# Optimization experiments

Hardware: AMD Instinct MI355X
Metric: run time of the kernel (lower is better)

## Reference

```python
import jax, jax.numpy as jnp
import numpy as np

EPS = 1e-5


def _layernorm(x, w, b):
    mu = jnp.mean(x, axis=-1, keepdims=True)
    xc = x - mu
    var = jnp.mean(xc * xc, axis=-1, keepdims=True)
    return xc * jax.lax.rsqrt(var + EPS) * w + b


def _s5_ssm(u, lam_re, lam_im, log_step, B_re, B_im, C_re, C_im, Dvec):
    # u: [B,L,D]; diagonal complex SSM with ZOH discretization + associative scan
    Lam = lam_re + 1j * lam_im                      # [P]
    step = jnp.exp(log_step)                        # [P]
    Abar = jnp.exp(Lam * step)                      # [P]
    Bbar = ((Abar - 1.0) / Lam)[:, None] * (B_re + 1j * B_im)  # [P,D]
    Bu = jnp.einsum('bld,pd->blp', u.astype(jnp.complex64), Bbar)  # [B,L,P]
    A_el = jnp.broadcast_to(Abar, Bu.shape)

    def binop(e1, e2):
        a1, b1 = e1
        a2, b2 = e2
        return a1 * a2, a2 * b1 + b2

    _, xs = jax.lax.associative_scan(binop, (A_el, Bu), axis=1)  # [B,L,P] complex
    y = jnp.einsum('blp,dp->bld', xs, C_re + 1j * C_im).real + Dvec * u
    return y


def _s5_block(x, an_w, an_b, lam_re, lam_im, log_step, B_re, B_im, C_re, C_im,
              Dvec, fn_w, fn_b, Wenc, Wdec):
    fx = _layernorm(x, an_w, an_b)
    s = _s5_ssm(fx, lam_re, lam_im, log_step, B_re, B_im, C_re, C_im, Dvec)
    z = jax.nn.gelu(s, approximate=False) + fx
    fy = _layernorm(z, fn_w, fn_b)
    h = fy @ Wenc.T                                  # [B,L,2D]
    a, g = jnp.split(h, 2, axis=-1)                  # GEGLU
    return (a * jax.nn.gelu(g, approximate=False)) @ Wdec.T + fy


def setup_inputs() -> dict:
    D = 1048   # d_model
    P = 1048   # state_dim
    NL = 3
    Bsz, L = 4, 4096
    key = jax.random.key(0)
    ks = jax.random.split(key, 20)
    f32 = jnp.float32
    inp = {}
    inp['x'] = jax.random.normal(ks[0], (Bsz, L, 1), f32)
    inp['enc_w'] = jax.random.normal(ks[1], (D, 1), f32)
    inp['enc_b'] = jnp.zeros((D,), f32)
    inp['norm_w'] = jnp.ones((NL, D), f32)
    inp['norm_b'] = jnp.zeros((NL, D), f32)
    inp['attn_norm_w'] = jnp.ones((NL, D), f32)
    inp['attn_norm_b'] = jnp.zeros((NL, D), f32)
    inp['ff_norm_w'] = jnp.ones((NL, D), f32)
    inp['ff_norm_b'] = jnp.zeros((NL, D), f32)
    # stable diagonal dynamics: Re(Lambda) < 0
    inp['lam_re'] = -0.5 * jax.random.uniform(ks[2], (NL, P), f32) - 0.05
    inp['lam_im'] = np.float32(np.pi) * jax.random.normal(ks[3], (NL, P), f32)
    lo, hi = np.float32(np.log(1e-3)), np.float32(np.log(1e-1))
    inp['log_step'] = lo + (hi - lo) * jax.random.uniform(ks[4], (NL, P), f32)
    sB = np.float32(1.0 / np.sqrt(D))
    sC = np.float32(1.0 / np.sqrt(P))
    inp['B_re'] = sB * jax.random.normal(ks[5], (NL, P, D), f32)
    inp['B_im'] = sB * jax.random.normal(ks[6], (NL, P, D), f32)
    inp['C_re'] = sC * jax.random.normal(ks[7], (NL, D, P), f32)
    inp['C_im'] = sC * jax.random.normal(ks[8], (NL, D, P), f32)
    inp['Dvec'] = jax.random.normal(ks[9], (NL, D), f32)
    sW = np.float32(1.0 / np.sqrt(D))
    inp['Wenc'] = sW * jax.random.normal(ks[10], (NL, 2 * D, D), f32)
    inp['Wdec'] = sW * jax.random.normal(ks[11], (NL, D, D), f32)
    inp['head_w'] = sW * jax.random.normal(ks[12], (1, D), f32)
    inp['head_b'] = jnp.zeros((1,), f32)
    return inp


def reference(x, enc_w, enc_b, norm_w, norm_b, attn_norm_w, attn_norm_b,
              ff_norm_w, ff_norm_b, lam_re, lam_im, log_step, B_re, B_im,
              C_re, C_im, Dvec, Wenc, Wdec, head_w, head_b):
    h = x @ enc_w.T + enc_b                          # [B,L,D]
    n_layers = norm_w.shape[0]
    for i in range(n_layers):                        # small fixed loop over layers
        z = _layernorm(h, norm_w[i], norm_b[i])      # prenorm
        z = _s5_block(z, attn_norm_w[i], attn_norm_b[i], lam_re[i], lam_im[i],
                      log_step[i], B_re[i], B_im[i], C_re[i], C_im[i],
                      Dvec[i], ff_norm_w[i], ff_norm_b[i], Wenc[i], Wdec[i])
        h = h + z                                    # residual (dropout = identity in eval)
    pooled = jnp.mean(h, axis=1)                     # [B,D]
    y = (pooled @ head_w.T + head_b).squeeze(-1)     # [B]
    return y
```

## Files before the change

kernel.cpp:

```cpp
#include <hip/hip_runtime.h>
#include <hip/hip_bf16.h>
#include <cstddef>

typedef __hip_bfloat16 bf16;

#define D_MODEL 1048
#define P_DIM   1048
#define NLAYER  3
#define BSZ     4
#define LSEQ    4096
#define BL      (BSZ*LSEQ)
#define BLD     ((size_t)BL*D_MODEL)
#define KP      1056
#define NP      1152
#define BLA     ((size_t)BL*KP)
#define NPKP    ((size_t)NP*KP)

#define NC      64
#define CL      (LSEQ/NC)
#define NSCAN   (BSZ*NC*P_DIM)
#define P2      (P_DIM/2)
#define NSCAN2  (BSZ*NC*P2)

typedef __attribute__((ext_vector_type(8))) short short8;
typedef __attribute__((ext_vector_type(4))) float f32x4;

#define BM 256
#define BN 128
#define TK 32
#define ASH (BM*TK)
#define BSH (BN*TK)
#define SLOT1 (ASH + BSH)
#define SLOT2 (ASH + 2*BSH)
#define KSTEPS  (KP/TK)
#define NG2   ((BL/BM)*(NP/BN))

__device__ __forceinline__ float gelu_f(float x) {
    return 0.5f * x * (1.f + erff(x * 0.70710678118654752f));
}

__device__ __forceinline__ void tile_coords(int id, int& m0, int& n0) {
    int xcd  = id & 7;
    int slot = id >> 3;
    int xg   = slot / 9;
    int j    = slot - xg*9;
    m0 = (xg*8 + xcd) * BM;
    n0 = j * BN;
}

__device__ __forceinline__ void stageA256(
    const bf16* __restrict__ src, int row0, int k0, short* lds, int tid)
{
#pragma unroll
    for (int c0 = 0; c0 < 2; ++c0) {
        int c = tid + 512*c0;
        int r = c >> 2;
        int col = ((c ^ (r >> 1)) & 3) * 8;
        __builtin_amdgcn_global_load_lds(
            (const __attribute__((address_space(1))) void*)(src + (size_t)(row0 + r)*KP + k0 + col),
            (__attribute__((address_space(3))) void*)(lds + c*8), 16, 0, 0);
    }
}
__device__ __forceinline__ void stageB128(
    const bf16* __restrict__ src, int row0, int k0, short* lds, int tid)
{
    int r = tid >> 2;
    int col = ((tid ^ (r >> 1)) & 3) * 8;
    __builtin_amdgcn_global_load_lds(
        (const __attribute__((address_space(1))) void*)(src + (size_t)(row0 + r)*KP + k0 + col),
        (__attribute__((address_space(3))) void*)(lds + tid*8), 16, 0, 0);
}

__device__ __forceinline__ void mfma_step1(
    const short* As, const short* Ws, f32x4 (&acc)[4][4],
    int wm, int wn, int row_in, int qs)
{
    short8 a[4], b[4];
#pragma unroll
    for (int i = 0; i < 4; ++i) {
        a[i] = *(const short8*)&As[(wm + i*16 + row_in)*TK + qs];
        b[i] = *(const short8*)&Ws[(wn + i*16 + row_in)*TK + qs];
    }
#pragma unroll
    for (int i = 0; i < 4; ++i)
#pragma unroll
        for (int j = 0; j < 4; ++j)
            acc[i][j] = __builtin_amdgcn_mfma_f32_16x16x32_bf16(a[i], b[j], acc[i][j], 0, 0, 0);
}

__device__ __forceinline__ void mfma_step2(
    const short* As, const short* W0s, const short* W1s,
    f32x4 (&acc0)[4][4], f32x4 (&acc1)[4][4],
    int wm, int wn, int row_in, int qs)
{
    short8 a[4], b0[4], b1[4];
#pragma unroll
    for (int i = 0; i < 4; ++i) {
        a[i]  = *(const short8*)&As [(wm + i*16 + row_in)*TK + qs];
        b0[i] = *(const short8*)&W0s[(wn + i*16 + row_in)*TK + qs];
        b1[i] = *(const short8*)&W1s[(wn + i*16 + row_in)*TK + qs];
    }
#pragma unroll
    for (int i = 0; i < 4; ++i)
#pragma unroll
        for (int j = 0; j < 4; ++j) {
            acc0[i][j] = __builtin_amdgcn_mfma_f32_16x16x32_bf16(a[i], b0[j], acc0[i][j], 0, 0, 0);
            acc1[i][j] = __builtin_amdgcn_mfma_f32_16x16x32_bf16(a[i], b1[j], acc1[i][j], 0, 0, 0);
        }
}

template <int NPASS>
__device__ __forceinline__ void kloop1(
    const bf16* __restrict__ A0, const bf16* __restrict__ W0,
    const bf16* __restrict__ A1, const bf16* __restrict__ W1,
    int m0, int n0, short* sm,
    f32x4 (&acc)[4][4], int tid, int wm, int wn, int row_in, int qs)
{
    const int NST = NPASS*KSTEPS;
#define STAGE1(t) { int _t = (t); \
        const bf16* _A = (NPASS == 2 && _t >= KSTEPS) ? A1 : A0; \
        const bf16* _W = (NPASS == 2 && _t >= KSTEPS) ? W1 : W0; \
        int _kk = (NPASS == 2 && _t >= KSTEPS) ? _t - KSTEPS : _t; \
        short* _b = sm + (_t & 3)*SLOT1; \
        stageA256(_A, m0, _kk*TK, _b, tid); \
        stageB128(_W, n0, _kk*TK, _b + ASH, tid); }
    STAGE1(0); STAGE1(1); STAGE1(2);
    for (int s = 0; s < NST; ++s) {
        if (s < NST - 2)       asm volatile("s_waitcnt vmcnt(6)" ::: "memory");
        else if (s == NST - 2) asm volatile("s_waitcnt vmcnt(3)" ::: "memory");
        else                   asm volatile("s_waitcnt vmcnt(0)" ::: "memory");
        __builtin_amdgcn_s_barrier();
        if (s < NST - 3) STAGE1(s + 3);
        short* base = sm + (s & 3)*SLOT1;
        __builtin_amdgcn_s_setprio(1);
        mfma_step1(base, base + ASH, acc, wm, wn, row_in, qs);
        __builtin_amdgcn_s_setprio(0);
    }
#undef STAGE1
}

template <int MODE>
__global__ __launch_bounds__(512, 2) void gemm2_k(
    const bf16* __restrict__ A, const bf16* __restrict__ W0,
    const bf16* __restrict__ W1,
    bf16* __restrict__ O0, bf16* __restrict__ O1, int N)
{
    __shared__ __align__(16) short sm[4*SLOT2];
    const int tid  = threadIdx.x;
    int m0, n0;
    tile_coords(blockIdx.x, m0, n0);
    const int wave = tid >> 6, lane = tid & 63;
    const int wm = (wave >> 1) * 64, wn = (wave & 1) * 64;
    const int row_in = lane & 15;
    const int qs = (((lane >> 4) ^ (lane >> 1)) & 3) * 8;

    f32x4 acc0[4][4] = {};
    f32x4 acc1[4][4] = {};

#define STAGE2(t) { int _t = (t); \
        short* _b = sm + (_t & 3)*SLOT2; \
        stageA256(A,  m0, _t*TK, _b, tid); \
        stageB128(W0, n0, _t*TK, _b + ASH, tid); \
        stageB128(W1, n0, _t*TK, _b + ASH + BSH, tid); }
    STAGE2(0); STAGE2(1); STAGE2(2);
    for (int s = 0; s < KSTEPS; ++s) {
        if (s < KSTEPS - 2)       asm volatile("s_waitcnt vmcnt(8)" ::: "memory");
        else if (s == KSTEPS - 2) asm volatile("s_waitcnt vmcnt(4)" ::: "memory");
        else                      asm volatile("s_waitcnt vmcnt(0)" ::: "memory");
        __builtin_amdgcn_s_barrier();
        if (s < KSTEPS - 3) STAGE2(s + 3);
        short* base = sm + (s & 3)*SLOT2;
        __builtin_amdgcn_s_setprio(1);
        mfma_step2(base, base + ASH, base + ASH + BSH, acc0, acc1, wm, wn, row_in, qs);
        __builtin_amdgcn_s_setprio(0);
    }
#undef STAGE2

    const int quad = lane >> 4;
#pragma unroll
    for (int i = 0; i < 4; ++i) {
#pragma unroll
        for (int j = 0; j < 4; ++j) {
            int n = n0 + wn + j*16 + row_in;
#pragma unroll
            for (int r = 0; r < 4; ++r) {
                int m = m0 + wm + i*16 + quad*4 + r;
                size_t o = (size_t)m*KP + n;
                if (MODE == 0) {
                    if (n < N)        { O0[o] = __float2bfloat16(acc0[i][j][r]);
                                        O1[o] = __float2bfloat16(acc1[i][j][r]); }
                    else if (n < KP)  { O0[o] = __float2bfloat16(0.f);
                                        O1[o] = __float2bfloat16(0.f); }
                } else {
                    if (n < N)        O0[o] = __float2bfloat16(acc0[i][j][r] * gelu_f(acc1[i][j][r]));
                    else if (n < KP)  O0[o] = __float2bfloat16(0.f);
                }
            }
        }
    }
}

__global__ __launch_bounds__(512, 2) void gemmC_k(
    const bf16* __restrict__ A0, const bf16* __restrict__ W0,
    const bf16* __restrict__ A1, const bf16* __restrict__ W1,
    const bf16* __restrict__ fx, const float* __restrict__ dv,
    bf16* __restrict__ O, int N)
{
    __shared__ __align__(16) short sm[4*SLOT1];
    const int tid  = threadIdx.x;
    int m0, n0;
    tile_coords(blockIdx.x, m0, n0);
    const int wave = tid >> 6, lane = tid & 63;
    const int wm = (wave >> 1) * 64, wn = (wave & 1) * 64;
    const int row_in = lane & 15;
    const int qs = (((lane >> 4) ^ (lane >> 1)) & 3) * 8;

    f32x4 acc[4][4] = {};
    kloop1<2>(A0, W0, A1, W1, m0, n0, sm, acc, tid, wm, wn, row_in, qs);

    const int quad = lane >> 4;
#pragma unroll
    for (int i = 0; i < 4; ++i) {
#pragma unroll
        for (int j = 0; j < 4; ++j) {
            int n = n0 + wn + j*16 + row_in;
#pragma unroll
            for (int r = 0; r < 4; ++r) {
                int m = m0 + wm + i*16 + quad*4 + r;
                size_t o = (size_t)m*KP + n;
                if (n < N) {
                    float f = __bfloat162float(fx[o]);
                    float t = acc[i][j][r] + dv[n]*f;
                    O[o] = __float2bfloat16(gelu_f(t) + f);
                } else if (n < KP) {
                    O[o] = __float2bfloat16(0.f);
                }
            }
        }
    }
}

__global__ __launch_bounds__(512, 2) void gemmD_k(
    const bf16* __restrict__ A, const bf16* __restrict__ W,
    const bf16* __restrict__ fy, float* __restrict__ h, int N)
{
    __shared__ __align__(16) short sm[4*SLOT1];
    const int tid  = threadIdx.x;
    int m0, n0;
    tile_coords(blockIdx.x, m0, n0);
    const int wave = tid >> 6, lane = tid & 63;
    const int wm = (wave >> 1) * 64, wn = (wave & 1) * 64;
    const int row_in = lane & 15;
    const int qs = (((lane >> 4) ^ (lane >> 1)) & 3) * 8;

    f32x4 acc[4][4] = {};
    kloop1<1>(A, W, nullptr, nullptr, m0, n0, sm, acc, tid, wm, wn, row_in, qs);

    const int quad = lane >> 4;
#pragma unroll
    for (int i = 0; i < 4; ++i) {
#pragma unroll
        for (int j = 0; j < 4; ++j) {
            int n = n0 + wn + j*16 + row_in;
            if (n >= N) continue;
#pragma unroll
            for (int r = 0; r < 4; ++r) {
                int m = m0 + wm + i*16 + quad*4 + r;
                float f = __bfloat162float(fy[(size_t)m*KP + n]);
                h[(size_t)m*D_MODEL + n] += acc[i][j][r] + f;
            }
        }
    }
}

__global__ __launch_bounds__(256) void convw5_k(
    const float* __restrict__ s0, const float* __restrict__ s1,
    const float* __restrict__ s2, const float* __restrict__ s3,
    const float* __restrict__ s4, bf16* __restrict__ dst)
{
    size_t i = (size_t)blockIdx.x*256 + threadIdx.x;
    if (i >= NPKP) return;
    int z = blockIdx.z;
    const float* src = (z == 0) ? s0 : (z == 1) ? s1 : (z == 2) ? s2 : (z == 3) ? s3 : s4;
    float scale = (z == 1) ? -1.f : 1.f;
    int n = (int)(i / KP), k = (int)(i - (size_t)n*KP);
    float v = (n < D_MODEL && k < D_MODEL) ? scale*src[(size_t)n*D_MODEL + k] : 0.f;
    dst[(size_t)z*NPKP + i] = __float2bfloat16(v);
}

__device__ __forceinline__ float2 block_reduce2(float a, float b) {
    __syncthreads();
    for (int off = 32; off; off >>= 1) {
        a += __shfl_down(a, off, 64);
        b += __shfl_down(b, off, 64);
    }
    __shared__ float sa[4], sb[4];
    int lane = threadIdx.x & 63, wv = threadIdx.x >> 6;
    if (lane == 0) { sa[wv] = a; sb[wv] = b; }
    __syncthreads();
    if (threadIdx.x == 0) {
        sa[0] = sa[0]+sa[1]+sa[2]+sa[3];
        sb[0] = sb[0]+sb[1]+sb[2]+sb[3];
    }
    __syncthreads();
    return make_float2(sa[0], sb[0]);
}

template <int ENC>
__global__ __launch_bounds__(256) void ln2x_k(
    const float* __restrict__ xin,
    const float* __restrict__ ew, const float* __restrict__ eb,
    float* __restrict__ hbuf,
    const float* __restrict__ w1, const float* __restrict__ bb1,
    const float* __restrict__ w2, const float* __restrict__ bb2,
    bf16* __restrict__ y)
{
    const size_t row = blockIdx.x;
    float v[5];
    float s = 0.f, ss = 0.f;
    int i = 0;
    if (ENC) {
        float xv = xin[row];
        float* hr = hbuf + row * D_MODEL;
        for (int d = threadIdx.x; d < KP; d += 256, ++i) {
            float t = 0.f;
            if (d < D_MODEL) { t = xv*ew[d] + eb[d]; hr[d] = t; }
            v[i] = t; s += t; ss += t*t;
        }
    } else {
        const float* xr = hbuf + row * D_MODEL;
        for (int d = threadIdx.x; d < KP; d += 256, ++i) {
            float t = (d < D_MODEL) ? xr[d] : 0.f;
            v[i] = t; s += t; ss += t*t;
        }
    }
    float2 r = block_reduce2(s, ss);
    float mu  = r.x * (1.f/D_MODEL);
    float var = r.y * (1.f/D_MODEL) - mu*mu;
    float inv = rsqrtf(var + 1e-5f);
    s = 0.f; ss = 0.f; i = 0;
    for (int d = threadIdx.x; d < KP; d += 256, ++i) {
        float z = (d < D_MODEL) ? (v[i]-mu)*inv*w1[d] + bb1[d] : 0.f;
        v[i] = z; s += z; ss += z*z;
    }
    r = block_reduce2(s, ss);
    mu  = r.x * (1.f/D_MODEL);
    var = r.y * (1.f/D_MODEL) - mu*mu;
    inv = rsqrtf(var + 1e-5f);
    bf16* yr = y + row * KP;
    i = 0;
    for (int d = threadIdx.x; d < KP; d += 256, ++i) {
        float o = (d < D_MODEL) ? (v[i]-mu)*inv*w2[d] + bb2[d] : 0.f;
        yr[d] = __float2bfloat16(o);
    }
}

__global__ __launch_bounds__(256) void ln_k(
    const bf16* __restrict__ x, const float* __restrict__ w,
    const float* __restrict__ b, bf16* __restrict__ y)
{
    const size_t row = blockIdx.x;
    const bf16* xr = x + row * KP;
    float v[5];
    float s = 0.f, ss = 0.f;
    int i = 0;
    for (int d = threadIdx.x; d < KP; d += 256, ++i) {
        float t = (d < D_MODEL) ? __bfloat162float(xr[d]) : 0.f;
        v[i] = t; s += t; ss += t*t;
    }
    float2 r = block_reduce2(s, ss);
    float mu  = r.x * (1.f/D_MODEL);
    float var = r.y * (1.f/D_MODEL) - mu*mu;
    float inv = rsqrtf(var + 1e-5f);
    bf16* yr = y + row * KP;
    i = 0;
    for (int d = threadIdx.x; d < KP; d += 256, ++i) {
        float o = (d < D_MODEL) ? (v[i]-mu)*inv*w[d] + b[d] : 0.f;
        yr[d] = __float2bfloat16(o);
    }
}

__global__ __launch_bounds__(256) void prep_k(
    const float* __restrict__ lam_re, const float* __restrict__ lam_im,
    const float* __restrict__ log_step,
    const float* __restrict__ B_re, const float* __restrict__ B_im,
    bf16* __restrict__ bbar_re, bf16* __restrict__ bbar_im,
    float* __restrict__ abar)
{
    size_t idx = (size_t)blockIdx.x*256 + threadIdx.x;
    if (idx >= NPKP) return;
    int p = (int)(idx / KP);
    int d = (int)(idx - (size_t)p*KP);
    if (p >= P_DIM || d >= D_MODEL) {
        bbar_re[idx] = __float2bfloat16(0.f);
        bbar_im[idx] = __float2bfloat16(0.f);
        return;
    }
    float lr = lam_re[p], li = lam_im[p];
    float st = expf(log_step[p]);
    float er = expf(lr*st);
    float ar = er * cosf(li*st);
    float ai = er * sinf(li*st);
    if (d == 0) { abar[p] = ar; abar[P_DIM + p] = ai; }
    float den = lr*lr + li*li;
    float xr = ar - 1.f, xi = ai;
    float cr = (xr*lr + xi*li) / den;
    float ci = (xi*lr - xr*li) / den;
    float br = B_re[(size_t)p*D_MODEL + d], bi = B_im[(size_t)p*D_MODEL + d];
    bbar_re[idx] = __float2bfloat16(cr*br - ci*bi);
    bbar_im[idx] = __float2bfloat16(cr*bi + ci*br);
}

__device__ __forceinline__ float2 bf2f(unsigned int u) {
    unsigned int lo = u << 16, hi = u & 0xffff0000u;
    float2 r;
    r.x = __uint_as_float(lo);
    r.y = __uint_as_float(hi);
    return r;
}
__device__ __forceinline__ unsigned int f2bf2(float a, float b) {
    bf16 ba = __float2bfloat16(a), bb = __float2bfloat16(b);
    unsigned short ua = *(unsigned short*)&ba, ub = *(unsigned short*)&bb;
    return (unsigned int)ua | ((unsigned int)ub << 16);
}

__global__ __launch_bounds__(256) void scan_partial_k(
    const unsigned int* __restrict__ ur, const unsigned int* __restrict__ ui,
    const float* __restrict__ abar,
    float* __restrict__ sum_re, float* __restrict__ sum_im)
{
    int idx = blockIdx.x*256 + threadIdx.x;
    if (idx >= NSCAN2) return;
    int p2 = idx % P2;
    int rest = idx / P2;
    int c = rest % NC, b = rest / NC;
    int p = 2*p2;
    float ar0 = abar[p],   ai0 = abar[P_DIM + p];
    float ar1 = abar[p+1], ai1 = abar[P_DIM + p + 1];
    size_t base = (((size_t)b*LSEQ + (size_t)c*CL)*KP + p) >> 1;
    float s0r = 0.f, s0i = 0.f, s1r = 0.f, s1i = 0.f;
    for (int i = 0; i < CL; ++i) {
        size_t o = base + (size_t)i*(KP/2);
        float2 br = bf2f(ur[o]);
        float2 bi = bf2f(ui[o]);
        float n0r = fmaf(ar0, s0r, fmaf(-ai0, s0i, br.x));
        float n0i = fmaf(ar0, s0i, fmaf( ai0, s0r, bi.x));
        float n1r = fmaf(ar1, s1r, fmaf(-ai1, s1i, br.y));
        float n1i = fmaf(ar1, s1i, fmaf( ai1, s1r, bi.y));
        s0r = n0r; s0i = n0i; s1r = n1r; s1i = n1i;
    }
    size_t so = ((size_t)b*NC + c)*P_DIM + p;
    *(float2*)&sum_re[so] = make_float2(s0r, s1r);
    *(float2*)&sum_im[so] = make_float2(s0i, s1i);
}

__global__ __launch_bounds__(256) void scan_carry_k(
    const float* __restrict__ sum_re, const float* __restrict__ sum_im,
    const float* __restrict__ abar,
    float* __restrict__ car_re, float* __restrict__ car_im)
{
    int idx = blockIdx.x*256 + threadIdx.x;
    if (idx >= BSZ*P_DIM) return;
    int p = idx % P_DIM, b = idx / P_DIM;
    float cr = abar[p], ci = abar[P_DIM + p];
#pragma unroll
    for (int s = 0; s < 6; ++s) {
        float nr = cr*cr - ci*ci;
        float ni = 2.f*cr*ci;
        cr = nr; ci = ni;
    }
    float xre = 0.f, xim = 0.f;
    size_t base = (size_t)b*NC*P_DIM + p;
    for (int c = 0; c < NC; ++c) {
        size_t o = base + (size_t)c*P_DIM;
        car_re[o] = xre; car_im[o] = xim;
        float sre = sum_re[o], sim = sum_im[o];
        float nr = fmaf(cr, xre, fmaf(-ci, xim, sre));
        float ni = fmaf(cr, xim, fmaf( ci, xre, sim));
        xre = nr; xim = ni;
    }
}

__global__ __launch_bounds__(256) void scan_apply_k(
    unsigned int* __restrict__ ur, unsigned int* __restrict__ ui,
    const float* __restrict__ abar,
    const float* __restrict__ car_re, const float* __restrict__ car_im)
{
    int idx = blockIdx.x*256 + threadIdx.x;
    if (idx >= NSCAN2) return;
    int p2 = idx % P2;
    int rest = idx / P2;
    int c = rest % NC, b = rest / NC;
    int p = 2*p2;
    float ar0 = abar[p],   ai0 = abar[P_DIM + p];
    float ar1 = abar[p+1], ai1 = abar[P_DIM + p + 1];
    size_t co = ((size_t)b*NC + c)*P_DIM + p;
    float2 c_r = *(const float2*)&car_re[co];
    float2 c_i = *(const float2*)&car_im[co];
    float x0r = c_r.x, x0i = c_i.x, x1r = c_r.y, x1i = c_i.y;
    size_t base = (((size_t)b*LSEQ + (size_t)c*CL)*KP + p) >> 1;
    for (int i = 0; i < CL; ++i) {
        size_t o = base + (size_t)i*(KP/2);
        float2 br = bf2f(ur[o]);
        float2 bi = bf2f(ui[o]);
        float n0r = fmaf(ar0, x0r, fmaf(-ai0, x0i, br.x));
        float n0i = fmaf(ar0, x0i, fmaf( ai0, x0r, bi.x));
        float n1r = fmaf(ar1, x1r, fmaf(-ai1, x1i, br.y));
        float n1i = fmaf(ar1, x1i, fmaf( ai1, x1r, bi.y));
        x0r = n0r; x0i = n0i; x1r = n1r; x1i = n1i;
        ur[o] = f2bf2(x0r, x1r);
        ui[o] = f2bf2(x0i, x1i);
    }
}

__global__ void head_init_k(float* out, const float* hb)
{
    if (threadIdx.x < BSZ) out[threadIdx.x] = hb[0];
}

__global__ __launch_bounds__(256) void head_k(
    const float* __restrict__ h, const float* __restrict__ hw,
    float* __restrict__ out)
{
    int b = blockIdx.x;
    int chunk = blockIdx.y;
    const float* hb = h + ((size_t)b*LSEQ + (size_t)chunk*64)*D_MODEL;
    float s = 0.f;
    for (int l = 0; l < 64; ++l) {
        const float* hr = hb + (size_t)l*D_MODEL;
        for (int d = threadIdx.x; d < D_MODEL; d += 256)
            s += hr[d]*hw[d];
    }
    for (int off = 32; off; off >>= 1) s += __shfl_down(s, off, 64);
    __shared__ float sm[4];
    int lane = threadIdx.x & 63, wv = threadIdx.x >> 6;
    if (lane == 0) sm[wv] = s;
    __syncthreads();
    if (threadIdx.x == 0)
        atomicAdd(out + b, (sm[0]+sm[1]+sm[2]+sm[3]) * (1.f/LSEQ));
}

extern "C" void kernel_launch(void* const* d_in, const int* in_sizes, int n_in,
                              void* d_out, int out_size, void* d_ws, size_t ws_size,
                              hipStream_t stream)
{
    const float* x          = (const float*)d_in[0];
    const float* enc_w      = (const float*)d_in[1];
    const float* enc_b      = (const float*)d_in[2];
    const float* norm_w     = (const float*)d_in[3];
    const float* norm_b     = (const float*)d_in[4];
    const float* attn_w     = (const float*)d_in[5];
    const float* attn_b     = (const float*)d_in[6];
    const float* ff_w       = (const float*)d_in[7];
    const float* ff_b       = (const float*)d_in[8];
    const float* lam_re     = (const float*)d_in[9];
    const float* lam_im     = (const float*)d_in[10];
    const float* log_step   = (const float*)d_in[11];
    const float* B_re       = (const float*)d_in[12];
    const float* B_im       = (const float*)d_in[13];
    const float* C_re       = (const float*)d_in[14];
    const float* C_im       = (const float*)d_in[15];
    const float* Dvec       = (const float*)d_in[16];
    const float* Wenc       = (const float*)d_in[17];
    const float* Wdec       = (const float*)d_in[18];
    const float* head_w     = (const float*)d_in[19];
    const float* head_b     = (const float*)d_in[20];
    float* out = (float*)d_out;

    float* h    = (float*)d_ws;
    bf16*  b1   = (bf16*)(h + BLD);
    bf16*  b2   = b1 + BLA;
    bf16*  b3   = b2 + BLA;
    bf16*  b4   = b3 + BLA;
    bf16*  wbr  = b4 + BLA;
    bf16*  wbi  = wbr + NPKP;
    bf16*  w5   = wbi + NPKP;
    bf16*  wcr  = w5;
    bf16*  wci  = w5 + NPKP;
    bf16*  wea  = w5 + 2*NPKP;
    bf16*  weg  = w5 + 3*NPKP;
    bf16*  wd   = w5 + 4*NPKP;
    float* abar = (float*)(w5 + 5*NPKP);
    float* sum_re = abar + 2*P_DIM;
    float* sum_im = sum_re + NSCAN;
    float* car_re = sum_im + NSCAN;
    float* car_im = car_re + NSCAN;

    const int CV   = (int)((NPKP + 255)/256);
    const int SC_G = (NSCAN2 + 255)/256;
    const size_t pd = (size_t)P_DIM*D_MODEL;

    for (int i = 0; i < NLAYER; ++i) {
        prep_k<<<CV, 256, 0, stream>>>(
            lam_re + i*P_DIM, lam_im + i*P_DIM, log_step + i*P_DIM,
            B_re + i*pd, B_im + i*pd, wbr, wbi, abar);
        const float* WencA = Wenc + (size_t)i*2*pd;
        const float* WencG = WencA + pd;
        convw5_k<<<dim3(CV,1,5), 256, 0, stream>>>(
            C_re + i*pd, C_im + i*pd, WencA, WencG, Wdec + i*pd, w5);

        if (i == 0)
            ln2x_k<1><<<BL, 256, 0, stream>>>(x, enc_w, enc_b, h,
                norm_w + i*D_MODEL, norm_b + i*D_MODEL,
                attn_w + i*D_MODEL, attn_b + i*D_MODEL, b2);
        else
            ln2x_k<0><<<BL, 256, 0, stream>>>(nullptr, nullptr, nullptr, h,
                norm_w + i*D_MODEL, norm_b + i*D_MODEL,
                attn_w + i*D_MODEL, attn_b + i*D_MODEL, b2);

        gemm2_k<0><<<NG2, 512, 0, stream>>>(b2, wbr, wbi, b1, b3, P_DIM);

        scan_partial_k<<<SC_G, 256, 0, stream>>>((unsigned int*)b1, (unsigned int*)b3,
                                                 abar, sum_re, sum_im);
        scan_carry_k<<<(BSZ*P_DIM + 255)/256, 256, 0, stream>>>(sum_re, sum_im, abar, car_re, car_im);
        scan_apply_k<<<SC_G, 256, 0, stream>>>((unsigned int*)b1, (unsigned int*)b3,
                                               abar, car_re, car_im);

        gemmC_k<<<NG2, 512, 0, stream>>>(b1, wcr, b3, wci, b2, Dvec + i*D_MODEL, b4, D_MODEL);

        ln_k<<<BL, 256, 0, stream>>>(b4, ff_w + i*D_MODEL, ff_b + i*D_MODEL, b1);

        gemm2_k<1><<<NG2, 512, 0, stream>>>(b1, wea, weg, b2, nullptr, D_MODEL);

        gemmD_k<<<NG2, 512, 0, stream>>>(b2, wd, b1, h, D_MODEL);
    }

    head_init_k<<<1, 64, 0, stream>>>(out, head_b);
    head_k<<<dim3(BSZ, 64), 256, 0, stream>>>(h, head_w, out);
}
```

Before: 2.012 ms.

## Restructure GEMM k-loops into double-k, two-buffer pipelines with interleaved LDS reads

Rewrites the main loops of the three GEMM kernels. Each iteration now consumes two 32-wide k-slices held in one of two LDS buffer groups, and LDS fragment reads are split into halves interleaved with MFMA groups behind extra barriers. New global-to-LDS copies for the next pair of slices are issued mid-iteration, with a separate tail for the odd 33rd slice. The launch-bounds minimum of two blocks per CU is dropped, giving the compiler more register freedom at possible cost in occupancy, and the added barriers may cost synchronisation overhead.

```diff
diff --git a/kernel.cpp b/kernel.cpp
--- a/kernel.cpp
+++ b/kernel.cpp
@@ -27,13 +27,13 @@
 
 #define BM 256
 #define BN 128
-#define TK 32
-#define ASH (BM*TK)
-#define BSH (BN*TK)
-#define SLOT1 (ASH + BSH)
-#define SLOT2 (ASH + 2*BSH)
-#define KSTEPS  (KP/TK)
+#define TKS 32
+#define ASL (BM*TKS)
+#define BSL (BN*TKS)
+#define KSTEPS 33
 #define NG2   ((BL/BM)*(NP/BN))
+
+#define BAR() asm volatile("s_barrier" ::: "memory")
 
 __device__ __forceinline__ float gelu_f(float x) {
     return 0.5f * x * (1.f + erff(x * 0.70710678118654752f));
@@ -48,7 +48,7 @@
     n0 = j * BN;
 }
 
-__device__ __forceinline__ void stageA256(
+__device__ __forceinline__ void stageA(
     const bf16* __restrict__ src, int row0, int k0, short* lds, int tid)
 {
 #pragma unroll
@@ -61,7 +61,7 @@
             (__attribute__((address_space(3))) void*)(lds + c*8), 16, 0, 0);
     }
 }
-__device__ __forceinline__ void stageB128(
+__device__ __forceinline__ void stageB(
     const bf16* __restrict__ src, int row0, int k0, short* lds, int tid)
 {
     int r = tid >> 2;
@@ -71,81 +71,20 @@
         (__attribute__((address_space(3))) void*)(lds + tid*8), 16, 0, 0);
 }
 
-__device__ __forceinline__ void mfma_step1(
-    const short* As, const short* Ws, f32x4 (&acc)[4][4],
-    int wm, int wn, int row_in, int qs)
-{
-    short8 a[4], b[4];
-#pragma unroll
-    for (int i = 0; i < 4; ++i) {
-        a[i] = *(const short8*)&As[(wm + i*16 + row_in)*TK + qs];
-        b[i] = *(const short8*)&Ws[(wn + i*16 + row_in)*TK + qs];
-    }
-#pragma unroll
-    for (int i = 0; i < 4; ++i)
-#pragma unroll
-        for (int j = 0; j < 4; ++j)
-            acc[i][j] = __builtin_amdgcn_mfma_f32_16x16x32_bf16(a[i], b[j], acc[i][j], 0, 0, 0);
-}
-
-__device__ __forceinline__ void mfma_step2(
-    const short* As, const short* W0s, const short* W1s,
-    f32x4 (&acc0)[4][4], f32x4 (&acc1)[4][4],
-    int wm, int wn, int row_in, int qs)
-{
-    short8 a[4], b0[4], b1[4];
-#pragma unroll
-    for (int i = 0; i < 4; ++i) {
-        a[i]  = *(const short8*)&As [(wm + i*16 + row_in)*TK + qs];
-        b0[i] = *(const short8*)&W0s[(wn + i*16 + row_in)*TK + qs];
-        b1[i] = *(const short8*)&W1s[(wn + i*16 + row_in)*TK + qs];
-    }
-#pragma unroll
-    for (int i = 0; i < 4; ++i)
-#pragma unroll
-        for (int j = 0; j < 4; ++j) {
-            acc0[i][j] = __builtin_amdgcn_mfma_f32_16x16x32_bf16(a[i], b0[j], acc0[i][j], 0, 0, 0);
-            acc1[i][j] = __builtin_amdgcn_mfma_f32_16x16x32_bf16(a[i], b1[j], acc1[i][j], 0, 0, 0);
-        }
-}
-
-template <int NPASS>
-__device__ __forceinline__ void kloop1(
-    const bf16* __restrict__ A0, const bf16* __restrict__ W0,
-    const bf16* __restrict__ A1, const bf16* __restrict__ W1,
-    int m0, int n0, short* sm,
-    f32x4 (&acc)[4][4], int tid, int wm, int wn, int row_in, int qs)
-{
-    const int NST = NPASS*KSTEPS;
-#define STAGE1(t) { int _t = (t); \
-        const bf16* _A = (NPASS == 2 && _t >= KSTEPS) ? A1 : A0; \
-        const bf16* _W = (NPASS == 2 && _t >= KSTEPS) ? W1 : W0; \
-        int _kk = (NPASS == 2 && _t >= KSTEPS) ? _t - KSTEPS : _t; \
-        short* _b = sm + (_t & 3)*SLOT1; \
-        stageA256(_A, m0, _kk*TK, _b, tid); \
-        stageB128(_W, n0, _kk*TK, _b + ASH, tid); }
-    STAGE1(0); STAGE1(1); STAGE1(2);
-    for (int s = 0; s < NST; ++s) {
-        if (s < NST - 2)       asm volatile("s_waitcnt vmcnt(6)" ::: "memory");
-        else if (s == NST - 2) asm volatile("s_waitcnt vmcnt(3)" ::: "memory");
-        else                   asm volatile("s_waitcnt vmcnt(0)" ::: "memory");
-        __builtin_amdgcn_s_barrier();
-        if (s < NST - 3) STAGE1(s + 3);
-        short* base = sm + (s & 3)*SLOT1;
-        __builtin_amdgcn_s_setprio(1);
-        mfma_step1(base, base + ASH, acc, wm, wn, row_in, qs);
-        __builtin_amdgcn_s_setprio(0);
-    }
-#undef STAGE1
+__device__ __forceinline__ short8 rd(const short* p, int row, int qs) {
+    return *(const short8*)&p[row*TKS + qs];
+}
+__device__ __forceinline__ f32x4 MF(short8 a, short8 b, f32x4 c) {
+    return __builtin_amdgcn_mfma_f32_16x16x32_bf16(a, b, c, 0, 0, 0);
 }
 
 template <int MODE>
-__global__ __launch_bounds__(512, 2) void gemm2_k(
+__global__ __launch_bounds__(512) void gemm2_k(
     const bf16* __restrict__ A, const bf16* __restrict__ W0,
     const bf16* __restrict__ W1,
     bf16* __restrict__ O0, bf16* __restrict__ O1, int N)
 {
-    __shared__ __align__(16) short sm[4*SLOT2];
+    __shared__ __align__(16) short sm[2][2*ASL + 4*BSL];
     const int tid  = threadIdx.x;
     int m0, n0;
     tile_coords(blockIdx.x, m0, n0);
@@ -157,24 +96,112 @@
     f32x4 acc0[4][4] = {};
     f32x4 acc1[4][4] = {};
 
-#define STAGE2(t) { int _t = (t); \
-        short* _b = sm + (_t & 3)*SLOT2; \
-        stageA256(A,  m0, _t*TK, _b, tid); \
-        stageB128(W0, n0, _t*TK, _b + ASH, tid); \
-        stageB128(W1, n0, _t*TK, _b + ASH + BSH, tid); }
-    STAGE2(0); STAGE2(1); STAGE2(2);
-    for (int s = 0; s < KSTEPS; ++s) {
-        if (s < KSTEPS - 2)       asm volatile("s_waitcnt vmcnt(8)" ::: "memory");
-        else if (s == KSTEPS - 2) asm volatile("s_waitcnt vmcnt(4)" ::: "memory");
-        else                      asm volatile("s_waitcnt vmcnt(0)" ::: "memory");
-        __builtin_amdgcn_s_barrier();
-        if (s < KSTEPS - 3) STAGE2(s + 3);
-        short* base = sm + (s & 3)*SLOT2;
-        __builtin_amdgcn_s_setprio(1);
-        mfma_step2(base, base + ASH, base + ASH + BSH, acc0, acc1, wm, wn, row_in, qs);
-        __builtin_amdgcn_s_setprio(0);
-    }
-#undef STAGE2
+#define STG2(s, c) { int _s=(s); int _kk=_s*TKS; \
+    stageA(A,  m0, _kk, sm[c] + (_s&1)*ASL, tid); \
+    stageB(W0, n0, _kk, sm[c] + 2*ASL + (_s&1)*BSL, tid); \
+    stageB(W1, n0, _kk, sm[c] + 2*ASL + 2*BSL + (_s&1)*BSL, tid); }
+
+    STG2(0,0); STG2(1,0); STG2(2,1); STG2(3,1);
+
+    for (int t = 0; t < 16; ++t) {
+        const int c = t & 1;
+        const short* bA  = sm[c];
+        const short* bB0 = sm[c] + 2*ASL;
+        const short* bB1 = sm[c] + 2*ASL + 2*BSL;
+        if (t < 15) asm volatile("s_waitcnt vmcnt(8)" ::: "memory");
+        else        asm volatile("s_waitcnt vmcnt(4)" ::: "memory");
+        BAR();
+        short8 af[2][2], b0f[4][2], b1f[4][2];
+#pragma unroll
+        for (int j = 0; j < 4; ++j) {
+            b0f[j][0] = rd(bB0,       wn + j*16 + row_in, qs);
+            b0f[j][1] = rd(bB0 + BSL, wn + j*16 + row_in, qs);
+        }
+#pragma unroll
+        for (int i = 0; i < 2; ++i) {
+            af[i][0] = rd(bA,       wm + i*16 + row_in, qs);
+            af[i][1] = rd(bA + ASL, wm + i*16 + row_in, qs);
+        }
+        BAR();
+        __builtin_amdgcn_s_setprio(1);
+#pragma unroll
+        for (int i = 0; i < 2; ++i)
+#pragma unroll
+            for (int j = 0; j < 4; ++j) {
+                acc0[i][j] = MF(af[i][0], b0f[j][0], acc0[i][j]);
+                acc0[i][j] = MF(af[i][1], b0f[j][1], acc0[i][j]);
+            }
+        __builtin_amdgcn_s_setprio(0);
+#pragma unroll
+        for (int j = 0; j < 4; ++j) {
+            b1f[j][0] = rd(bB1,       wn + j*16 + row_in, qs);
+            b1f[j][1] = rd(bB1 + BSL, wn + j*16 + row_in, qs);
+        }
+        BAR();
+        __builtin_amdgcn_s_setprio(1);
+#pragma unroll
+        for (int i = 0; i < 2; ++i)
+#pragma unroll
+            for (int j = 0; j < 4; ++j) {
+                acc1[i][j] = MF(af[i][0], b1f[j][0], acc1[i][j]);
+                acc1[i][j] = MF(af[i][1], b1f[j][1], acc1[i][j]);
+            }
+        __builtin_amdgcn_s_setprio(0);
+        short8 ag[2][2];
+#pragma unroll
+        for (int i = 0; i < 2; ++i) {
+            ag[i][0] = rd(bA,       wm + (i+2)*16 + row_in, qs);
+            ag[i][1] = rd(bA + ASL, wm + (i+2)*16 + row_in, qs);
+        }
+        BAR();
+        if (t < 14)       { STG2(2*t+4, c); STG2(2*t+5, c); }
+        else if (t == 14) { STG2(32, 0); }
+        __builtin_amdgcn_s_setprio(1);
+#pragma unroll
+        for (int i = 0; i < 2; ++i)
+#pragma unroll
+            for (int j = 0; j < 4; ++j) {
+                acc0[i+2][j] = MF(ag[i][0], b0f[j][0], acc0[i+2][j]);
+                acc0[i+2][j] = MF(ag[i][1], b0f[j][1], acc0[i+2][j]);
+            }
+        __builtin_amdgcn_s_setprio(0);
+        BAR();
+        __builtin_amdgcn_s_setprio(1);
+#pragma unroll
+        for (int i = 0; i < 2; ++i)
+#pragma unroll
+            for (int j = 0; j < 4; ++j) {
+                acc1[i+2][j] = MF(ag[i][0], b1f[j][0], acc1[i+2][j]);
+                acc1[i+2][j] = MF(ag[i][1], b1f[j][1], acc1[i+2][j]);
+            }
+        __builtin_amdgcn_s_setprio(0);
+        BAR();
+    }
+#undef STG2
+    {
+        const short* bA  = sm[0];
+        const short* bB0 = sm[0] + 2*ASL;
+        const short* bB1 = sm[0] + 2*ASL + 2*BSL;
+        asm volatile("s_waitcnt vmcnt(0)" ::: "memory");
+        BAR();
+        short8 at[4], b0t[4], b1t[4];
+#pragma unroll
+        for (int i = 0; i < 4; ++i) at[i] = rd(bA, wm + i*16 + row_in, qs);
+#pragma unroll
+        for (int j = 0; j < 4; ++j) {
+            b0t[j] = rd(bB0, wn + j*16 + row_in, qs);
+            b1t[j] = rd(bB1, wn + j*16 + row_in, qs);
+        }
+        __builtin_amdgcn_s_setprio(1);
+#pragma unroll
+        for (int i = 0; i < 4; ++i)
+#pragma unroll
+            for (int j = 0; j < 4; ++j) {
+                acc0[i][j] = MF(at[i], b0t[j], acc0[i][j]);
+                acc1[i][j] = MF(at[i], b1t[j], acc1[i][j]);
+            }
+        __builtin_amdgcn_s_setprio(0);
+    }
 
     const int quad = lane >> 4;
 #pragma unroll
@@ -200,13 +227,13 @@
     }
 }
 
-__global__ __launch_bounds__(512, 2) void gemmC_k(
+__global__ __launch_bounds__(512) void gemmC_k(
     const bf16* __restrict__ A0, const bf16* __restrict__ W0,
     const bf16* __restrict__ A1, const bf16* __restrict__ W1,
     const bf16* __restrict__ fx, const float* __restrict__ dv,
     bf16* __restrict__ O, int N)
 {
-    __shared__ __align__(16) short sm[4*SLOT1];
+    __shared__ __align__(16) short sm[2][2*ASL + 2*BSL];
     const int tid  = threadIdx.x;
     int m0, n0;
     tile_coords(blockIdx.x, m0, n0);
@@ -216,7 +243,64 @@
     const int qs = (((lane >> 4) ^ (lane >> 1)) & 3) * 8;
 
     f32x4 acc[4][4] = {};
-    kloop1<2>(A0, W0, A1, W1, m0, n0, sm, acc, tid, wm, wn, row_in, qs);
+
+#define STGC(s, c) { int _s=(s); \
+    const bf16* _A = _s < KSTEPS ? A0 : A1; \
+    const bf16* _W = _s < KSTEPS ? W0 : W1; \
+    int _kk = (_s < KSTEPS ? _s : _s - KSTEPS)*TKS; \
+    stageA(_A, m0, _kk, sm[c] + (_s&1)*ASL, tid); \
+    stageB(_W, n0, _kk, sm[c] + 2*ASL + (_s&1)*BSL, tid); }
+
+    STGC(0,0); STGC(1,0); STGC(2,1); STGC(3,1);
+
+    for (int t = 0; t < 33; ++t) {
+        const int c = t & 1;
+        const short* bA = sm[c];
+        const short* bB = sm[c] + 2*ASL;
+        if (t < 32) asm volatile("s_waitcnt vmcnt(6)" ::: "memory");
+        else        asm volatile("s_waitcnt vmcnt(0)" ::: "memory");
+        BAR();
+        short8 bf[4][2], af[2][2];
+#pragma unroll
+        for (int j = 0; j < 4; ++j) {
+            bf[j][0] = rd(bB,       wn + j*16 + row_in, qs);
+            bf[j][1] = rd(bB + BSL, wn + j*16 + row_in, qs);
+        }
+#pragma unroll
+        for (int i = 0; i < 2; ++i) {
+            af[i][0] = rd(bA,       wm + i*16 + row_in, qs);
+            af[i][1] = rd(bA + ASL, wm + i*16 + row_in, qs);
+        }
+        BAR();
+        __builtin_amdgcn_s_setprio(1);
+#pragma unroll
+        for (int i = 0; i < 2; ++i)
+#pragma unroll
+            for (int j = 0; j < 4; ++j) {
+                acc[i][j] = MF(af[i][0], bf[j][0], acc[i][j]);
+                acc[i][j] = MF(af[i][1], bf[j][1], acc[i][j]);
+            }
+        __builtin_amdgcn_s_setprio(0);
+        short8 ag[2][2];
+#pragma unroll
+        for (int i = 0; i < 2; ++i) {
+            ag[i][0] = rd(bA,       wm + (i+2)*16 + row_in, qs);
+            ag[i][1] = rd(bA + ASL, wm + (i+2)*16 + row_in, qs);
+        }
+        BAR();
+        if (t < 31) { STGC(2*t+4, c); STGC(2*t+5, c); }
+        __builtin_amdgcn_s_setprio(1);
+#pragma unroll
+        for (int i = 0; i < 2; ++i)
+#pragma unroll
+            for (int j = 0; j < 4; ++j) {
+                acc[i+2][j] = MF(ag[i][0], bf[j][0], acc[i+2][j]);
+                acc[i+2][j] = MF(ag[i][1], bf[j][1], acc[i+2][j]);
+            }
+        __builtin_amdgcn_s_setprio(0);
+        BAR();
+    }
+#undef STGC
 
     const int quad = lane >> 4;
 #pragma unroll
@@ -230,8 +314,8 @@
                 size_t o = (size_t)m*KP + n;
                 if (n < N) {
                     float f = __bfloat162float(fx[o]);
-                    float t = acc[i][j][r] + dv[n]*f;
-                    O[o] = __float2bfloat16(gelu_f(t) + f);
+                    float t2 = acc[i][j][r] + dv[n]*f;
+                    O[o] = __float2bfloat16(gelu_f(t2) + f);
                 } else if (n < KP) {
                     O[o] = __float2bfloat16(0.f);
                 }
@@ -240,11 +324,11 @@
     }
 }
 
-__global__ __launch_bounds__(512, 2) void gemmD_k(
+__global__ __launch_bounds__(512) void gemmD_k(
     const bf16* __restrict__ A, const bf16* __restrict__ W,
     const bf16* __restrict__ fy, float* __restrict__ h, int N)
 {
-    __shared__ __align__(16) short sm[4*SLOT1];
+    __shared__ __align__(16) short sm[2][2*ASL + 2*BSL];
     const int tid  = threadIdx.x;
     int m0, n0;
     tile_coords(blockIdx.x, m0, n0);
@@ -254,7 +338,80 @@
     const int qs = (((lane >> 4) ^ (lane >> 1)) & 3) * 8;
 
     f32x4 acc[4][4] = {};
-    kloop1<1>(A, W, nullptr, nullptr, m0, n0, sm, acc, tid, wm, wn, row_in, qs);
+
+#define STGD(s, c) { int _s=(s); int _kk=_s*TKS; \
+    stageA(A, m0, _kk, sm[c] + (_s&1)*ASL, tid); \
+    stageB(W, n0, _kk, sm[c] + 2*ASL + (_s&1)*BSL, tid); }
+
+    STGD(0,0); STGD(1,0); STGD(2,1); STGD(3,1);
+
+    for (int t = 0; t < 16; ++t) {
+        const int c = t & 1;
+        const short* bA = sm[c];
+        const short* bB = sm[c] + 2*ASL;
+        if (t < 15) asm volatile("s_waitcnt vmcnt(6)" ::: "memory");
+        else        asm volatile("s_waitcnt vmcnt(3)" ::: "memory");
+        BAR();
+        short8 bf[4][2], af[2][2];
+#pragma unroll
+        for (int j = 0; j < 4; ++j) {
+            bf[j][0] = rd(bB,       wn + j*16 + row_in, qs);
+            bf[j][1] = rd(bB + BSL, wn + j*16 + row_in, qs);
+        }
+#pragma unroll
+        for (int i = 0; i < 2; ++i) {
+            af[i][0] = rd(bA,       wm + i*16 + row_in, qs);
+            af[i][1] = rd(bA + ASL, wm + i*16 + row_in, qs);
+        }
+        BAR();
+        __builtin_amdgcn_s_setprio(1);
+#pragma unroll
+        for (int i = 0; i < 2; ++i)
+#pragma unroll
+            for (int j = 0; j < 4; ++j) {
+                acc[i][j] = MF(af[i][0], bf[j][0], acc[i][j]);
+                acc[i][j] = MF(af[i][1], bf[j][1], acc[i][j]);
+            }
+        __builtin_amdgcn_s_setprio(0);
+        short8 ag[2][2];
+#pragma unroll
+        for (int i = 0; i < 2; ++i) {
+            ag[i][0] = rd(bA,       wm + (i+2)*16 + row_in, qs);
+            ag[i][1] = rd(bA + ASL, wm + (i+2)*16 + row_in, qs);
+        }
+        BAR();
+        if (t < 14)       { STGD(2*t+4, c); STGD(2*t+5, c); }
+        else if (t == 14) { STGD(32, 0); }
+        __builtin_amdgcn_s_setprio(1);
+#pragma unroll
+        for (int i = 0; i < 2; ++i)
+#pragma unroll
+            for (int j = 0; j < 4; ++j) {
+                acc[i+2][j] = MF(ag[i][0], bf[j][0], acc[i+2][j]);
+                acc[i+2][j] = MF(ag[i][1], bf[j][1], acc[i+2][j]);
+            }
+        __builtin_amdgcn_s_setprio(0);
+        BAR();
+    }
+#undef STGD
+    {
+        const short* bA = sm[0];
+        const short* bB = sm[0] + 2*ASL;
+        asm volatile("s_waitcnt vmcnt(0)" ::: "memory");
+        BAR();
+        short8 at[4], bt[4];
+#pragma unroll
+        for (int i = 0; i < 4; ++i) at[i] = rd(bA, wm + i*16 + row_in, qs);
+#pragma unroll
+        for (int j = 0; j < 4; ++j) bt[j] = rd(bB, wn + j*16 + row_in, qs);
+        __builtin_amdgcn_s_setprio(1);
+#pragma unroll
+        for (int i = 0; i < 4; ++i)
+#pragma unroll
+            for (int j = 0; j < 4; ++j)
+                acc[i][j] = MF(at[i], bt[j], acc[i][j]);
+        __builtin_amdgcn_s_setprio(0);
+    }
 
     const int quad = lane >> 4;
 #pragma unroll
```

Result: slower. 2.117 ms (+5.2%).
